# Kernel tuning notes

Hardware: AMD Instinct MI355X
Metric: run time of the kernel (lower is better)

## Reference

```python
import jax, jax.numpy as jnp
import numpy as np

B, N, DIM = 2, 512, 128
HEADS, DH = 4, 64
INNER = HEADS * DH            # 256
POS_HID = 64
MULT = 4                      # attn_mlp_hidden_mult
K = 16                        # num_neighbors


def setup_inputs() -> dict:
    key = jax.random.key(0)
    ks = jax.random.split(key, 10)
    w = lambda k, shape: jax.random.normal(k, shape, jnp.float32) * 0.02
    return {
        "x": jax.random.normal(ks[0], (B, N, DIM), jnp.float32),
        "pos": jax.random.normal(ks[1], (B, N, 3), jnp.float32),
        "mask": jnp.ones((B, N), dtype=bool),
        "w_qkv": w(ks[2], (DIM, 3 * INNER)),
        "w_out": w(ks[3], (INNER, DIM)),
        "b_out": jnp.zeros((DIM,), jnp.float32),
        "w_pos1": w(ks[4], (3, POS_HID)),
        "b_pos1": jnp.zeros((POS_HID,), jnp.float32),
        "w_pos2": w(ks[5], (POS_HID, INNER)),
        "b_pos2": jnp.zeros((INNER,), jnp.float32),
        # grouped 1x1 convs == per-head linear layers
        "w_attn1": w(ks[6], (HEADS, DH, MULT * DH)),
        "b_attn1": jnp.zeros((HEADS, MULT * DH), jnp.float32),
        "w_attn2": w(ks[7], (HEADS, MULT * DH, DH)),
        "b_attn2": jnp.zeros((HEADS, DH), jnp.float32),
    }


def reference(x, pos, mask, w_qkv, w_out, b_out, w_pos1, b_pos1, w_pos2, b_pos2,
              w_attn1, b_attn1, w_attn2, b_attn2):
    b, n, _ = x.shape
    h, d = HEADS, DH

    qkv = x @ w_qkv                                   # [b, n, 3*inner]
    q, k, v = jnp.split(qkv, 3, axis=-1)
    to_heads = lambda t: t.reshape(b, n, h, d).transpose(0, 2, 1, 3)  # b h n d
    q, k, v = map(to_heads, (q, k, v))

    # dense pairwise relative positions + pos MLP  [b, n, n, inner]
    rel_pos = pos[:, :, None, :] - pos[:, None, :, :]            # [b, n, n, 3]
    rpe = jax.nn.relu(rel_pos @ w_pos1 + b_pos1) @ w_pos2 + b_pos2

    # masked topk over pairwise distance (smallest K)
    rel_dist = jnp.linalg.norm(rel_pos, axis=-1)                 # [b, n, n]
    mask2 = mask[:, :, None] & mask[:, None, :]                  # [b, n, n]
    fmax = jnp.finfo(rel_dist.dtype).max
    rel_dist = jnp.where(mask2, rel_dist, fmax)
    _, idx = jax.lax.top_k(-rel_dist, K)                         # [b, n, K]

    # neighbor gathers (equivalent to torch batched_index_select over j)
    gather_hd = jax.vmap(lambda t, i: t[:, i, :])                # [h,n,d],[n,K] -> [h,n,K,d]
    k_nb = gather_hd(k, idx)                                     # [b, h, n, K, d]
    v_nb = gather_hd(v, idx)
    row = jnp.arange(n)[:, None]
    rpe_nb = jax.vmap(lambda r, i: r[row, i])(rpe, idx)          # [b, n, K, inner]
    rpe_nb = rpe_nb.reshape(b, n, K, h, d).transpose(0, 3, 1, 2, 4)  # [b,h,n,K,d]
    mask_nb = jax.vmap(lambda m, i: m[row, i])(mask2, idx)       # [b, n, K]

    # qk_rel gathered implicitly: (q_i - k_j)[j=idx] == q_i - k_nb
    attn_in = q[:, :, :, None, :] - k_nb + rpe_nb                # [b, h, n, K, d]

    # grouped 1x1 conv MLP == per-head MLP on last dim
    hid = jax.nn.relu(jnp.einsum('bhikd,hde->bhike', attn_in, w_attn1)
                      + b_attn1[None, :, None, None, :])
    sim = (jnp.einsum('bhike,hed->bhikd', hid, w_attn2)
           + b_attn2[None, :, None, None, :])                    # [b, h, n, K, d]

    sim = jnp.where(mask_nb[:, None, :, :, None], sim, -fmax)
    # torch: sim is [b, (h d), i, j]; softmax(dim=-2) is over i -> axis 2 here
    attn = jax.nn.softmax(sim, axis=2)

    v_full = v_nb + rpe_nb                                       # [b, h, n, K, d]
    agg = jnp.sum(attn * v_full, axis=3)                         # [b, h, n, d]
    agg = agg.transpose(0, 2, 1, 3).reshape(b, n, h * d)         # [b, n, inner]
    return agg @ w_out + b_out
```

## Files before the change

kernel.cpp:

```cpp
#include <hip/hip_runtime.h>

#define B_ 2
#define N_ 512
#define DIM_ 128
#define HEADS_ 4
#define DH_ 64
#define INNER_ 256
#define PH_ 64
#define HID2_ 256
#define KNB_ 16

typedef unsigned long long u64;
typedef unsigned int u32;
typedef unsigned short u16;
typedef __attribute__((ext_vector_type(8))) short bf16x8;
typedef __attribute__((ext_vector_type(8))) unsigned short us8;
typedef __attribute__((ext_vector_type(4))) float f32x4;

__device__ __forceinline__ float bf2f(u16 u) {
    union { float f; u32 u; } c; c.u = ((u32)u) << 16; return c.f;
}
__device__ __forceinline__ u16 f2bf(float f) {
    union { float f; u32 u; } c; c.f = f;
    u32 u = c.u;
    return (u16)((u + 0x7fffu + ((u >> 16) & 1u)) >> 16);
}
__device__ __forceinline__ u32 pack2(float lo, float hi) {
    return ((u32)f2bf(hi) << 16) | (u32)f2bf(lo);
}

__global__ __launch_bounds__(256) void k_front(
        const float* __restrict__ x, const float* __restrict__ pos, const float* __restrict__ w_qkv,
        const float* __restrict__ w_a1, const float* __restrict__ w_a2, const float* __restrict__ w_p2,
        u16* __restrict__ wf1, u16* __restrict__ wf2, u16* __restrict__ wfp,
        u16* __restrict__ qb, u16* __restrict__ kb, float* __restrict__ v,
        int* __restrict__ idx) {
    int blk = blockIdx.x;
    if (blk < 576) {
        int t = blk * 256 + threadIdx.x;
        if (t < 65536) {
            int jj = t & 7, lbig = (t >> 3) & 63, f = t >> 9;
            int s = f & 1, etL = (f >> 1) & 7, half = (f >> 4) & 1, h = f >> 5;
            int lr = lbig & 15, g = lbig >> 4;
            int d = s * 32 + g * 8 + jj, e = (half * 8 + etL) * 16 + lr;
            wf1[t] = f2bf(w_a1[((h * 64 + d) << 8) + e]);
        } else if (t < 131072) {
            int t2 = t - 65536;
            int jj = t2 & 7, lbig = (t2 >> 3) & 63, f = t2 >> 9;
            int s = f & 7, ct = (f >> 3) & 3, h = f >> 5;
            int lr = lbig & 15, g = lbig >> 4;
            int e = s * 32 + g * 8 + jj, c = ct * 16 + lr;
            wf2[t2] = f2bf(w_a2[(((h << 8) + e) << 6) + c]);
        } else {
            int t3 = t - 131072;
            int jj = t3 & 7, lbig = (t3 >> 3) & 63, f = t3 >> 9;
            int s = f & 1, ct = (f >> 1) & 3, h = f >> 3;
            int lr = lbig & 15, g = lbig >> 4;
            int e = s * 32 + g * 8 + jj, c = h * 64 + ct * 16 + lr;
            wfp[t3] = f2bf(w_p2[(e << 8) + c]);
        }
    } else if (blk < 704) {
        int bu = blk - 576;
        int b = bu >> 6;
        int n0 = (bu & 63) * 8;
        int t = threadIdx.x;
        __shared__ float xs[8][128];
        #pragma unroll
        for (int p = 0; p < 4; ++p) {
            int e = p * 256 + t;
            xs[e >> 7][e & 127] = x[((size_t)(b * N_ + n0) + (e >> 7)) * DIM_ + (e & 127)];
        }
        __syncthreads();
        float acc[3][8];
        #pragma unroll
        for (int cc = 0; cc < 3; ++cc)
            #pragma unroll
            for (int r = 0; r < 8; ++r) acc[cc][r] = 0.f;
        for (int c4 = 0; c4 < 32; ++c4) {
            float wv[3][4];
            #pragma unroll
            for (int dd = 0; dd < 4; ++dd)
                #pragma unroll
                for (int cc = 0; cc < 3; ++cc)
                    wv[cc][dd] = w_qkv[(size_t)(c4 * 4 + dd) * (3 * INNER_) + cc * INNER_ + t];
            #pragma unroll
            for (int r = 0; r < 8; ++r) {
                float4 xv = *(const float4*)&xs[r][c4 * 4];
                #pragma unroll
                for (int cc = 0; cc < 3; ++cc)
                    acc[cc][r] += xv.x * wv[cc][0] + xv.y * wv[cc][1] + xv.z * wv[cc][2] + xv.w * wv[cc][3];
            }
        }
        int h = t >> 6, d = t & 63;
        #pragma unroll
        for (int r = 0; r < 8; ++r) {
            size_t o = (((size_t)(b * HEADS_ + h)) * N_ + n0 + r) * DH_ + d;
            qb[o] = f2bf(acc[0][r]);
            kb[o] = f2bf(acc[1][r]);
            v[o]  = acc[2][r];
        }
    } else {
        int wave = (blk - 704) * 4 + (threadIdx.x >> 6);
        int lane = threadIdx.x & 63;
        int b = wave >> 9;
        float px = pos[(size_t)wave * 3 + 0];
        float py = pos[(size_t)wave * 3 + 1];
        float pz = pos[(size_t)wave * 3 + 2];
        u64 keys[8];
        #pragma unroll
        for (int s = 0; s < 8; ++s) {
            int j = s * 64 + lane;
            float dx = __fsub_rn(px, pos[(size_t)(b * N_ + j) * 3 + 0]);
            float dy = __fsub_rn(py, pos[(size_t)(b * N_ + j) * 3 + 1]);
            float dz = __fsub_rn(pz, pos[(size_t)(b * N_ + j) * 3 + 2]);
            float s2 = __fadd_rn(__fadd_rn(__fmul_rn(dx, dx), __fmul_rn(dy, dy)), __fmul_rn(dz, dz));
            float dist = __fsqrt_rn(s2);
            keys[s] = ((u64)__float_as_uint(dist) << 32) | (unsigned)j;
        }
        for (int r = 0; r < KNB_; ++r) {
            u64 m = keys[0];
            #pragma unroll
            for (int s = 1; s < 8; ++s) m = (keys[s] < m) ? keys[s] : m;
            #pragma unroll
            for (int off = 32; off >= 1; off >>= 1) {
                u64 o = __shfl_xor(m, off);
                m = (o < m) ? o : m;
            }
            if (lane == 0) idx[(size_t)wave * KNB_ + r] = (int)(m & 0xffffffffu);
            #pragma unroll
            for (int s = 0; s < 8; ++s) if (keys[s] == m) keys[s] = ~0ull;
        }
    }
}

__global__ __launch_bounds__(256, 2) void k_gather(
        const u16* __restrict__ qb, const u16* __restrict__ kb, const float* __restrict__ v,
        const int* __restrict__ idx, const float* __restrict__ pos,
        const float* __restrict__ w_p1, const float* __restrict__ b_p1,
        const float* __restrict__ b_p2, const u16* __restrict__ wfp,
        u16* __restrict__ ainb, u16* __restrict__ vf) {
    __shared__ u16 RP[4][2][16 * 72];
    int t = threadIdx.x;
    int wv = t >> 6, l = t & 63, lr = l & 15, g = l >> 4;
    int blk = blockIdx.x;
    int b = blk >> 8;
    int i0 = (blk & 255) * 2;
    int h = wv, bh = b * HEADS_ + h;

    float rx[2], ry[2], rz[2];
    us8 qv[2][2], kv[2][2];
    float4 v0[2][2], v1[2][2];
    #pragma unroll
    for (int ii = 0; ii < 2; ++ii) {
        int i = i0 + ii, bi = (b << 9) + i;
        int j = idx[(bi << 4) + lr];
        int bj = (b << 9) + j;
        rx[ii] = pos[(size_t)bi * 3 + 0] - pos[(size_t)bj * 3 + 0];
        ry[ii] = pos[(size_t)bi * 3 + 1] - pos[(size_t)bj * 3 + 1];
        rz[ii] = pos[(size_t)bi * 3 + 2] - pos[(size_t)bj * 3 + 2];
        #pragma unroll
        for (int s = 0; s < 2; ++s) {
            qv[ii][s] = *(const us8*)&qb[(size_t)(bh * N_ + i) * 64 + s * 32 + g * 8];
            kv[ii][s] = *(const us8*)&kb[(size_t)(bh * N_ + j) * 64 + s * 32 + g * 8];
            v0[ii][s] = *(const float4*)&v[(size_t)(bh * N_ + j) * 64 + s * 32 + g * 8];
            v1[ii][s] = *(const float4*)&v[(size_t)(bh * N_ + j) * 64 + s * 32 + g * 8 + 4];
        }
    }

    bf16x8 hidp[2][2];
    #pragma unroll
    for (int ii = 0; ii < 2; ++ii) {
        #pragma unroll
        for (int s = 0; s < 2; ++s) {
            u16 tmp[8];
            #pragma unroll
            for (int jj = 0; jj < 8; ++jj) {
                int e = s * 32 + g * 8 + jj;
                float hh = b_p1[e] + rx[ii] * w_p1[e] + ry[ii] * w_p1[PH_ + e] + rz[ii] * w_p1[2 * PH_ + e];
                tmp[jj] = f2bf(fmaxf(hh, 0.f));
            }
            hidp[ii][s] = *(bf16x8*)tmp;
        }
    }

    {
        bf16x8 Ar[4][2];
        #pragma unroll
        for (int ct = 0; ct < 4; ++ct)
            #pragma unroll
            for (int s = 0; s < 2; ++s)
                Ar[ct][s] = *(const bf16x8*)&wfp[(size_t)((((h << 2) + ct) << 1) + s) * 512 + l * 8];
        #pragma unroll
        for (int ct = 0; ct < 4; ++ct) {
            f32x4 C0 = {0.f, 0.f, 0.f, 0.f}, C1 = {0.f, 0.f, 0.f, 0.f};
            #pragma unroll
            for (int s = 0; s < 2; ++s) {
                C0 = __builtin_amdgcn_mfma_f32_16x16x32_bf16(Ar[ct][s], hidp[0][s], C0, 0, 0, 0);
                C1 = __builtin_amdgcn_mfma_f32_16x16x32_bf16(Ar[ct][s], hidp[1][s], C1, 0, 0, 0);
            }
            float4 bias = *(const float4*)&b_p2[h * 64 + ct * 16 + g * 4];
            uint2 o0, o1;
            o0.x = pack2(C0[0] + bias.x, C0[1] + bias.y);
            o0.y = pack2(C0[2] + bias.z, C0[3] + bias.w);
            o1.x = pack2(C1[0] + bias.x, C1[1] + bias.y);
            o1.y = pack2(C1[2] + bias.z, C1[3] + bias.w);
            *(uint2*)&RP[wv][0][lr * 72 + ct * 16 + g * 4] = o0;
            *(uint2*)&RP[wv][1][lr * 72 + ct * 16 + g * 4] = o1;
        }
    }

    #pragma unroll
    for (int ii = 0; ii < 2; ++ii) {
        int i = i0 + ii;
        #pragma unroll
        for (int s = 0; s < 2; ++s) {
            bf16x8 rp = *(const bf16x8*)&RP[wv][ii][lr * 72 + s * 32 + g * 8];
            us8 rpu = *(const us8*)&rp;
            float vvr[8] = {v0[ii][s].x, v0[ii][s].y, v0[ii][s].z, v0[ii][s].w,
                            v1[ii][s].x, v1[ii][s].y, v1[ii][s].z, v1[ii][s].w};
            u16 ta[8], tv[8];
            #pragma unroll
            for (int jj = 0; jj < 8; ++jj) {
                float rpf = bf2f(rpu[jj]);
                ta[jj] = f2bf(bf2f(qv[ii][s][jj]) - bf2f(kv[ii][s][jj]) + rpf);
                tv[jj] = f2bf(vvr[jj] + rpf);
            }
            *(bf16x8*)&ainb[((size_t)((bh * N_ + i) * 2 + s)) * 512 + l * 8] = *(bf16x8*)ta;
            *(bf16x8*)&vf[(size_t)(((bh * N_ + i) << 4) + lr) * 64 + s * 32 + g * 8] = *(bf16x8*)tv;
        }
    }
}

__global__ __launch_bounds__(256, 2) void k_mlp(
        const u16* __restrict__ ainb,
        const u16* __restrict__ wf1, const u16* __restrict__ wf2,
        const float* __restrict__ b_a1, const float* __restrict__ b_a2,
        u16* __restrict__ sim) {
    __shared__ u16 HID[4][2][16 * 136];
    int t = threadIdx.x;
    int wv = t >> 6, l = t & 63, lr = l & 15, g = l >> 4;
    int blk = blockIdx.x;
    int bh = blk >> 6;
    int h = bh & 3;
    int i0 = (blk & 63) * 8 + wv * 2;

    bf16x8 ain[2][2];
    #pragma unroll
    for (int ii = 0; ii < 2; ++ii) {
        int i = i0 + ii;
        #pragma unroll
        for (int s = 0; s < 2; ++s)
            ain[ii][s] = *(const bf16x8*)&ainb[((size_t)((bh * N_ + i) * 2 + s)) * 512 + l * 8];
    }

    f32x4 C2[2][4];
    #pragma unroll
    for (int ii = 0; ii < 2; ++ii)
        #pragma unroll
        for (int ct = 0; ct < 4; ++ct) C2[ii][ct] = (f32x4){0.f, 0.f, 0.f, 0.f};
    #pragma unroll
    for (int half = 0; half < 2; ++half) {
        bf16x8 A1[8][2];
        #pragma unroll
        for (int etL = 0; etL < 8; ++etL)
            #pragma unroll
            for (int s = 0; s < 2; ++s)
                A1[etL][s] = *(const bf16x8*)&wf1[(size_t)(((((h << 1) + half) << 3) + etL) * 2 + s) * 512 + l * 8];
        #pragma unroll
        for (int etL = 0; etL < 8; ++etL) {
            int et = half * 8 + etL;
            f32x4 C0 = {0.f, 0.f, 0.f, 0.f}, C1 = {0.f, 0.f, 0.f, 0.f};
            #pragma unroll
            for (int s = 0; s < 2; ++s) {
                C0 = __builtin_amdgcn_mfma_f32_16x16x32_bf16(A1[etL][s], ain[0][s], C0, 0, 0, 0);
                C1 = __builtin_amdgcn_mfma_f32_16x16x32_bf16(A1[etL][s], ain[1][s], C1, 0, 0, 0);
            }
            float4 bias = *(const float4*)&b_a1[h * 256 + et * 16 + g * 4];
            uint2 p0, p1;
            p0.x = pack2(fmaxf(C0[0] + bias.x, 0.f), fmaxf(C0[1] + bias.y, 0.f));
            p0.y = pack2(fmaxf(C0[2] + bias.z, 0.f), fmaxf(C0[3] + bias.w, 0.f));
            p1.x = pack2(fmaxf(C1[0] + bias.x, 0.f), fmaxf(C1[1] + bias.y, 0.f));
            p1.y = pack2(fmaxf(C1[2] + bias.z, 0.f), fmaxf(C1[3] + bias.w, 0.f));
            *(uint2*)&HID[wv][0][lr * 136 + etL * 16 + g * 4] = p0;
            *(uint2*)&HID[wv][1][lr * 136 + etL * 16 + g * 4] = p1;
        }
        #pragma unroll
        for (int chunk = 0; chunk < 2; ++chunk) {
            bf16x8 A2[4][2];
            #pragma unroll
            for (int ct = 0; ct < 4; ++ct)
                #pragma unroll
                for (int ss = 0; ss < 2; ++ss) {
                    int s = half * 4 + chunk * 2 + ss;
                    A2[ct][ss] = *(const bf16x8*)&wf2[(size_t)((((h << 2) + ct) << 3) + s) * 512 + l * 8];
                }
            #pragma unroll
            for (int ss = 0; ss < 2; ++ss) {
                int sL = chunk * 2 + ss;
                bf16x8 B0 = *(const bf16x8*)&HID[wv][0][lr * 136 + sL * 32 + g * 8];
                bf16x8 B1 = *(const bf16x8*)&HID[wv][1][lr * 136 + sL * 32 + g * 8];
                #pragma unroll
                for (int ct = 0; ct < 4; ++ct) {
                    C2[0][ct] = __builtin_amdgcn_mfma_f32_16x16x32_bf16(A2[ct][ss], B0, C2[0][ct], 0, 0, 0);
                    C2[1][ct] = __builtin_amdgcn_mfma_f32_16x16x32_bf16(A2[ct][ss], B1, C2[1][ct], 0, 0, 0);
                }
            }
        }
    }
    #pragma unroll
    for (int ii = 0; ii < 2; ++ii) {
        int i = i0 + ii;
        #pragma unroll
        for (int ct = 0; ct < 4; ++ct) {
            float4 bias = *(const float4*)&b_a2[h * 64 + ct * 16 + g * 4];
            uint2 o;
            o.x = pack2(C2[ii][ct][0] + bias.x, C2[ii][ct][1] + bias.y);
            o.y = pack2(C2[ii][ct][2] + bias.z, C2[ii][ct][3] + bias.w);
            *(uint2*)&sim[(size_t)(((bh * N_ + i) << 4) + lr) * 64 + ct * 16 + g * 4] = o;
        }
    }
}

__global__ __launch_bounds__(256) void k_stats(const u16* __restrict__ sim, float* __restrict__ P) {
    int blk = blockIdx.x;
    int half = blk & 1, ks = (blk >> 1) & 15, bh = blk >> 5;
    int d0 = (threadIdx.x & 15) * 4;
    int nc = threadIdx.x >> 4;
    __shared__ float red[16][69];
    size_t base = ((size_t)(bh * N_ + half * 256 + nc * 16) * 16 + ks) * 64 + d0;
    float s0 = 0.f, s1 = 0.f, s2 = 0.f, s3 = 0.f;
    #pragma unroll
    for (int nn = 0; nn < 16; ++nn) {
        uint2 u = *(const uint2*)&sim[base + (size_t)nn * 1024];
        s0 += __expf(bf2f((u16)(u.x & 0xffff)));
        s1 += __expf(bf2f((u16)(u.x >> 16)));
        s2 += __expf(bf2f((u16)(u.y & 0xffff)));
        s3 += __expf(bf2f((u16)(u.y >> 16)));
    }
    red[nc][d0 + 0] = s0; red[nc][d0 + 1] = s1;
    red[nc][d0 + 2] = s2; red[nc][d0 + 3] = s3;
    __syncthreads();
    int t = threadIdx.x;
    if (t < 64) {
        float s = 0.f;
        #pragma unroll
        for (int c = 0; c < 16; ++c) s += red[c][t];
        P[(size_t)blk * 64 + t] = s;
    }
}

__global__ __launch_bounds__(256) void k_agg_out(
        const u16* __restrict__ sim, const u16* __restrict__ vf, const float* __restrict__ P,
        const float* __restrict__ w, const float* __restrict__ bo, float* __restrict__ out) {
    int blk = blockIdx.x;
    int b = blk >> 8;
    int i0 = (blk & 255) * 2;
    int t = threadIdx.x;
    __shared__ float ag[2][260];
    {
        int h = t >> 6, d = t & 63;
        int bh = b * HEADS_ + h;
        float Rk[16];
        #pragma unroll
        for (int ks = 0; ks < 16; ++ks) {
            int pbase = ((bh << 5) + (ks << 1)) * 64 + d;
            Rk[ks] = 1.f / (P[pbase] + P[pbase + 64]);
        }
        #pragma unroll
        for (int r = 0; r < 2; ++r) {
            size_t base = (size_t)((bh * N_ + i0 + r) << 4) * 64 + d;
            float acc = 0.f;
            #pragma unroll
            for (int ks = 0; ks < 16; ++ks) {
                float p = __expf(bf2f(sim[base + (size_t)ks * 64])) * Rk[ks];
                acc += p * bf2f(vf[base + (size_t)ks * 64]);
            }
            ag[r][h * 64 + d] = acc;
        }
    }
    __syncthreads();
    int c = t & 127, rg = t >> 7;
    float acc = bo[c];
    for (int k4 = 0; k4 < 64; ++k4) {
        float4 a4 = *(const float4*)&ag[rg][k4 * 4];
        acc += a4.x * w[(size_t)(k4 * 4 + 0) * DIM_ + c] + a4.y * w[(size_t)(k4 * 4 + 1) * DIM_ + c]
             + a4.z * w[(size_t)(k4 * 4 + 2) * DIM_ + c] + a4.w * w[(size_t)(k4 * 4 + 3) * DIM_ + c];
    }
    out[(size_t)((b << 9) + i0 + rg) * DIM_ + c] = acc;
}

extern "C" void kernel_launch(void* const* d_in, const int* in_sizes, int n_in,
                              void* d_out, int out_size, void* d_ws, size_t ws_size,
                              hipStream_t stream) {
    const float* x      = (const float*)d_in[0];
    const float* pos    = (const float*)d_in[1];
    const float* w_qkv  = (const float*)d_in[3];
    const float* w_out  = (const float*)d_in[4];
    const float* b_out  = (const float*)d_in[5];
    const float* w_pos1 = (const float*)d_in[6];
    const float* b_pos1 = (const float*)d_in[7];
    const float* w_pos2 = (const float*)d_in[8];
    const float* b_pos2 = (const float*)d_in[9];
    const float* w_a1   = (const float*)d_in[10];
    const float* b_a1   = (const float*)d_in[11];
    const float* w_a2   = (const float*)d_in[12];
    const float* b_a2   = (const float*)d_in[13];
    float* out = (float*)d_out;

    char* W = (char*)d_ws;
    u16*  qb   = (u16*)W;            W += 524288;
    u16*  kb   = (u16*)W;            W += 524288;
    float* v   = (float*)W;          W += 1048576;
    int*  idx  = (int*)W;            W += 65536;
    u16*  sim  = (u16*)W;            W += 8388608;
    u16*  vf   = (u16*)W;            W += 8388608;
    u16*  ainb = (u16*)W;            W += 8388608;
    float* P   = (float*)W;          W += 65536;
    u16*  wf1  = (u16*)W;            W += 131072;
    u16*  wf2  = (u16*)W;            W += 131072;
    u16*  wfp  = (u16*)W;            W += 32768;

    k_front<<<960, 256, 0, stream>>>(x, pos, w_qkv, w_a1, w_a2, w_pos2,
                                     wf1, wf2, wfp, qb, kb, v, idx);
    k_gather<<<512, 256, 0, stream>>>(qb, kb, v, idx, pos, w_pos1, b_pos1, b_pos2, wfp,
                                      ainb, vf);
    k_mlp<<<512, 256, 0, stream>>>(ainb, wf1, wf2, b_a1, b_a2, sim);
    k_stats<<<256, 256, 0, stream>>>(sim, P);
    k_agg_out<<<512, 256, 0, stream>>>(sim, vf, P, w_out, b_out, out);
}
```

Before: 56.56 us.

## Fuse gather and attention-MLP kernels, keep attn input in registers, store V as bf16

Merges k_gather and k_mlp into a single k_attn kernel. The attention-MLP input is now kept in registers instead of being written to and re-read from an 8 MB global buffer, and the extra launch goes away. The block mapping changes so each block covers one (batch, head) pair with 8 query rows, and the LDS buffer is reused for both the rpe tile and the hidden activations. V is also stored as bf16 instead of fp32, halving its traffic, at some precision cost in v+rpe.

```diff
diff --git a/kernel.cpp b/kernel.cpp
--- a/kernel.cpp
+++ b/kernel.cpp
@@ -33,7 +33,7 @@
         const float* __restrict__ x, const float* __restrict__ pos, const float* __restrict__ w_qkv,
         const float* __restrict__ w_a1, const float* __restrict__ w_a2, const float* __restrict__ w_p2,
         u16* __restrict__ wf1, u16* __restrict__ wf2, u16* __restrict__ wfp,
-        u16* __restrict__ qb, u16* __restrict__ kb, float* __restrict__ v,
+        u16* __restrict__ qb, u16* __restrict__ kb, u16* __restrict__ vb,
         int* __restrict__ idx) {
     int blk = blockIdx.x;
     if (blk < 576) {
@@ -97,7 +97,7 @@
             size_t o = (((size_t)(b * HEADS_ + h)) * N_ + n0 + r) * DH_ + d;
             qb[o] = f2bf(acc[0][r]);
             kb[o] = f2bf(acc[1][r]);
-            v[o]  = acc[2][r];
+            vb[o] = f2bf(acc[2][r]);
         }
     } else {
         int wave = (blk - 704) * 4 + (threadIdx.x >> 6);
@@ -133,23 +133,24 @@
     }
 }
 
-__global__ __launch_bounds__(256, 2) void k_gather(
-        const u16* __restrict__ qb, const u16* __restrict__ kb, const float* __restrict__ v,
-        const int* __restrict__ idx, const float* __restrict__ pos,
-        const float* __restrict__ w_p1, const float* __restrict__ b_p1,
+__global__ __launch_bounds__(256, 2) void k_attn(
+        const u16* __restrict__ qb, const u16* __restrict__ kb, const u16* __restrict__ vb,
+        const int* __restrict__ idx,
+        const float* __restrict__ pos, const float* __restrict__ w_p1, const float* __restrict__ b_p1,
         const float* __restrict__ b_p2, const u16* __restrict__ wfp,
-        u16* __restrict__ ainb, u16* __restrict__ vf) {
-    __shared__ u16 RP[4][2][16 * 72];
+        const u16* __restrict__ wf1, const u16* __restrict__ wf2,
+        const float* __restrict__ b_a1, const float* __restrict__ b_a2,
+        u16* __restrict__ sim, u16* __restrict__ vf) {
+    __shared__ u16 HID[4][2][16 * 136];
     int t = threadIdx.x;
     int wv = t >> 6, l = t & 63, lr = l & 15, g = l >> 4;
     int blk = blockIdx.x;
-    int b = blk >> 8;
-    int i0 = (blk & 255) * 2;
-    int h = wv, bh = b * HEADS_ + h;
+    int bh = blk >> 6;
+    int b = bh >> 2, h = bh & 3;
+    int i0 = (blk & 63) * 8 + wv * 2;
 
     float rx[2], ry[2], rz[2];
-    us8 qv[2][2], kv[2][2];
-    float4 v0[2][2], v1[2][2];
+    us8 qv[2][2], kv[2][2], vvb[2][2];
     #pragma unroll
     for (int ii = 0; ii < 2; ++ii) {
         int i = i0 + ii, bi = (b << 9) + i;
@@ -160,10 +161,9 @@
         rz[ii] = pos[(size_t)bi * 3 + 2] - pos[(size_t)bj * 3 + 2];
         #pragma unroll
         for (int s = 0; s < 2; ++s) {
-            qv[ii][s] = *(const us8*)&qb[(size_t)(bh * N_ + i) * 64 + s * 32 + g * 8];
-            kv[ii][s] = *(const us8*)&kb[(size_t)(bh * N_ + j) * 64 + s * 32 + g * 8];
-            v0[ii][s] = *(const float4*)&v[(size_t)(bh * N_ + j) * 64 + s * 32 + g * 8];
-            v1[ii][s] = *(const float4*)&v[(size_t)(bh * N_ + j) * 64 + s * 32 + g * 8 + 4];
+            qv[ii][s]  = *(const us8*)&qb[(size_t)(bh * N_ + i) * 64 + s * 32 + g * 8];
+            kv[ii][s]  = *(const us8*)&kb[(size_t)(bh * N_ + j) * 64 + s * 32 + g * 8];
+            vvb[ii][s] = *(const us8*)&vb[(size_t)(bh * N_ + j) * 64 + s * 32 + g * 8];
         }
     }
 
@@ -204,53 +204,29 @@
             o0.y = pack2(C0[2] + bias.z, C0[3] + bias.w);
             o1.x = pack2(C1[0] + bias.x, C1[1] + bias.y);
             o1.y = pack2(C1[2] + bias.z, C1[3] + bias.w);
-            *(uint2*)&RP[wv][0][lr * 72 + ct * 16 + g * 4] = o0;
-            *(uint2*)&RP[wv][1][lr * 72 + ct * 16 + g * 4] = o1;
-        }
-    }
-
+            *(uint2*)&HID[wv][0][lr * 136 + ct * 16 + g * 4] = o0;
+            *(uint2*)&HID[wv][1][lr * 136 + ct * 16 + g * 4] = o1;
+        }
+    }
+
+    bf16x8 ain[2][2];
     #pragma unroll
     for (int ii = 0; ii < 2; ++ii) {
         int i = i0 + ii;
         #pragma unroll
         for (int s = 0; s < 2; ++s) {
-            bf16x8 rp = *(const bf16x8*)&RP[wv][ii][lr * 72 + s * 32 + g * 8];
+            bf16x8 rp = *(const bf16x8*)&HID[wv][ii][lr * 136 + s * 32 + g * 8];
             us8 rpu = *(const us8*)&rp;
-            float vvr[8] = {v0[ii][s].x, v0[ii][s].y, v0[ii][s].z, v0[ii][s].w,
-                            v1[ii][s].x, v1[ii][s].y, v1[ii][s].z, v1[ii][s].w};
             u16 ta[8], tv[8];
             #pragma unroll
             for (int jj = 0; jj < 8; ++jj) {
                 float rpf = bf2f(rpu[jj]);
                 ta[jj] = f2bf(bf2f(qv[ii][s][jj]) - bf2f(kv[ii][s][jj]) + rpf);
-                tv[jj] = f2bf(vvr[jj] + rpf);
-            }
-            *(bf16x8*)&ainb[((size_t)((bh * N_ + i) * 2 + s)) * 512 + l * 8] = *(bf16x8*)ta;
+                tv[jj] = f2bf(bf2f(vvb[ii][s][jj]) + rpf);
+            }
+            ain[ii][s] = *(bf16x8*)ta;
             *(bf16x8*)&vf[(size_t)(((bh * N_ + i) << 4) + lr) * 64 + s * 32 + g * 8] = *(bf16x8*)tv;
         }
-    }
-}
-
-__global__ __launch_bounds__(256, 2) void k_mlp(
-        const u16* __restrict__ ainb,
-        const u16* __restrict__ wf1, const u16* __restrict__ wf2,
-        const float* __restrict__ b_a1, const float* __restrict__ b_a2,
-        u16* __restrict__ sim) {
-    __shared__ u16 HID[4][2][16 * 136];
-    int t = threadIdx.x;
-    int wv = t >> 6, l = t & 63, lr = l & 15, g = l >> 4;
-    int blk = blockIdx.x;
-    int bh = blk >> 6;
-    int h = bh & 3;
-    int i0 = (blk & 63) * 8 + wv * 2;
-
-    bf16x8 ain[2][2];
-    #pragma unroll
-    for (int ii = 0; ii < 2; ++ii) {
-        int i = i0 + ii;
-        #pragma unroll
-        for (int s = 0; s < 2; ++s)
-            ain[ii][s] = *(const bf16x8*)&ainb[((size_t)((bh * N_ + i) * 2 + s)) * 512 + l * 8];
     }
 
     f32x4 C2[2][4];
@@ -410,21 +386,19 @@
     char* W = (char*)d_ws;
     u16*  qb   = (u16*)W;            W += 524288;
     u16*  kb   = (u16*)W;            W += 524288;
-    float* v   = (float*)W;          W += 1048576;
+    u16*  vb   = (u16*)W;            W += 524288;
     int*  idx  = (int*)W;            W += 65536;
     u16*  sim  = (u16*)W;            W += 8388608;
     u16*  vf   = (u16*)W;            W += 8388608;
-    u16*  ainb = (u16*)W;            W += 8388608;
     float* P   = (float*)W;          W += 65536;
     u16*  wf1  = (u16*)W;            W += 131072;
     u16*  wf2  = (u16*)W;            W += 131072;
     u16*  wfp  = (u16*)W;            W += 32768;
 
     k_front<<<960, 256, 0, stream>>>(x, pos, w_qkv, w_a1, w_a2, w_pos2,
-                                     wf1, wf2, wfp, qb, kb, v, idx);
-    k_gather<<<512, 256, 0, stream>>>(qb, kb, v, idx, pos, w_pos1, b_pos1, b_pos2, wfp,
-                                      ainb, vf);
-    k_mlp<<<512, 256, 0, stream>>>(ainb, wf1, wf2, b_a1, b_a2, sim);
+                                     wf1, wf2, wfp, qb, kb, vb, idx);
+    k_attn<<<512, 256, 0, stream>>>(qb, kb, vb, idx, pos, w_pos1, b_pos1, b_pos2, wfp,
+                                    wf1, wf2, b_a1, b_a2, sim, vf);
     k_stats<<<256, 256, 0, stream>>>(sim, P);
     k_agg_out<<<512, 256, 0, stream>>>(sim, vf, P, w_out, b_out, out);
 }
```

Measured after the change: 59.64 us. +5.4%, slower.

## Stage MLP weights and positions in LDS, store V as bf16

Applied to the files above, without the earlier changes.

k_mlp now copies the per-head wf1/wf2 weight fragments (64 KB) into shared memory once per block and reads MFMA A operands from LDS instead of from global memory per wave. k_gather stages the batch's positions in shared memory for the relative-position computation. V is stored and gathered in bf16 instead of fp32, which halves its traffic. The exchange is a large LDS footprint in k_mlp, with the min-blocks launch bound dropped, which lowers occupancy, plus extra rounding of V.

```diff
diff --git a/kernel.cpp b/kernel.cpp
--- a/kernel.cpp
+++ b/kernel.cpp
@@ -33,7 +33,7 @@
         const float* __restrict__ x, const float* __restrict__ pos, const float* __restrict__ w_qkv,
         const float* __restrict__ w_a1, const float* __restrict__ w_a2, const float* __restrict__ w_p2,
         u16* __restrict__ wf1, u16* __restrict__ wf2, u16* __restrict__ wfp,
-        u16* __restrict__ qb, u16* __restrict__ kb, float* __restrict__ v,
+        u16* __restrict__ qb, u16* __restrict__ kb, u16* __restrict__ vb,
         int* __restrict__ idx) {
     int blk = blockIdx.x;
     if (blk < 576) {
@@ -97,7 +97,7 @@
             size_t o = (((size_t)(b * HEADS_ + h)) * N_ + n0 + r) * DH_ + d;
             qb[o] = f2bf(acc[0][r]);
             kb[o] = f2bf(acc[1][r]);
-            v[o]  = acc[2][r];
+            vb[o] = f2bf(acc[2][r]);
         }
     } else {
         int wave = (blk - 704) * 4 + (threadIdx.x >> 6);
@@ -134,12 +134,13 @@
 }
 
 __global__ __launch_bounds__(256, 2) void k_gather(
-        const u16* __restrict__ qb, const u16* __restrict__ kb, const float* __restrict__ v,
+        const u16* __restrict__ qb, const u16* __restrict__ kb, const u16* __restrict__ vb,
         const int* __restrict__ idx, const float* __restrict__ pos,
         const float* __restrict__ w_p1, const float* __restrict__ b_p1,
         const float* __restrict__ b_p2, const u16* __restrict__ wfp,
         u16* __restrict__ ainb, u16* __restrict__ vf) {
     __shared__ u16 RP[4][2][16 * 72];
+    __shared__ float PSM[1536];
     int t = threadIdx.x;
     int wv = t >> 6, l = t & 63, lr = l & 15, g = l >> 4;
     int blk = blockIdx.x;
@@ -147,36 +148,40 @@
     int i0 = (blk & 255) * 2;
     int h = wv, bh = b * HEADS_ + h;
 
-    float rx[2], ry[2], rz[2];
-    us8 qv[2][2], kv[2][2];
-    float4 v0[2][2], v1[2][2];
+    #pragma unroll
+    for (int p = 0; p < 6; ++p)
+        PSM[p * 256 + t] = pos[(size_t)b * 1536 + p * 256 + t];
+
+    int jn[2];
+    us8 qv[2][2], kv[2][2], vvb[2][2];
     #pragma unroll
     for (int ii = 0; ii < 2; ++ii) {
         int i = i0 + ii, bi = (b << 9) + i;
         int j = idx[(bi << 4) + lr];
-        int bj = (b << 9) + j;
-        rx[ii] = pos[(size_t)bi * 3 + 0] - pos[(size_t)bj * 3 + 0];
-        ry[ii] = pos[(size_t)bi * 3 + 1] - pos[(size_t)bj * 3 + 1];
-        rz[ii] = pos[(size_t)bi * 3 + 2] - pos[(size_t)bj * 3 + 2];
+        jn[ii] = j;
         #pragma unroll
         for (int s = 0; s < 2; ++s) {
-            qv[ii][s] = *(const us8*)&qb[(size_t)(bh * N_ + i) * 64 + s * 32 + g * 8];
-            kv[ii][s] = *(const us8*)&kb[(size_t)(bh * N_ + j) * 64 + s * 32 + g * 8];
-            v0[ii][s] = *(const float4*)&v[(size_t)(bh * N_ + j) * 64 + s * 32 + g * 8];
-            v1[ii][s] = *(const float4*)&v[(size_t)(bh * N_ + j) * 64 + s * 32 + g * 8 + 4];
-        }
-    }
+            qv[ii][s]  = *(const us8*)&qb[(size_t)(bh * N_ + i) * 64 + s * 32 + g * 8];
+            kv[ii][s]  = *(const us8*)&kb[(size_t)(bh * N_ + j) * 64 + s * 32 + g * 8];
+            vvb[ii][s] = *(const us8*)&vb[(size_t)(bh * N_ + j) * 64 + s * 32 + g * 8];
+        }
+    }
+    __syncthreads();
 
     bf16x8 hidp[2][2];
     #pragma unroll
     for (int ii = 0; ii < 2; ++ii) {
+        int i = i0 + ii, j = jn[ii];
+        float rx = PSM[i * 3 + 0] - PSM[j * 3 + 0];
+        float ry = PSM[i * 3 + 1] - PSM[j * 3 + 1];
+        float rz = PSM[i * 3 + 2] - PSM[j * 3 + 2];
         #pragma unroll
         for (int s = 0; s < 2; ++s) {
             u16 tmp[8];
             #pragma unroll
             for (int jj = 0; jj < 8; ++jj) {
                 int e = s * 32 + g * 8 + jj;
-                float hh = b_p1[e] + rx[ii] * w_p1[e] + ry[ii] * w_p1[PH_ + e] + rz[ii] * w_p1[2 * PH_ + e];
+                float hh = b_p1[e] + rx * w_p1[e] + ry * w_p1[PH_ + e] + rz * w_p1[2 * PH_ + e];
                 tmp[jj] = f2bf(fmaxf(hh, 0.f));
             }
             hidp[ii][s] = *(bf16x8*)tmp;
@@ -216,14 +221,12 @@
         for (int s = 0; s < 2; ++s) {
             bf16x8 rp = *(const bf16x8*)&RP[wv][ii][lr * 72 + s * 32 + g * 8];
             us8 rpu = *(const us8*)&rp;
-            float vvr[8] = {v0[ii][s].x, v0[ii][s].y, v0[ii][s].z, v0[ii][s].w,
-                            v1[ii][s].x, v1[ii][s].y, v1[ii][s].z, v1[ii][s].w};
             u16 ta[8], tv[8];
             #pragma unroll
             for (int jj = 0; jj < 8; ++jj) {
                 float rpf = bf2f(rpu[jj]);
                 ta[jj] = f2bf(bf2f(qv[ii][s][jj]) - bf2f(kv[ii][s][jj]) + rpf);
-                tv[jj] = f2bf(vvr[jj] + rpf);
+                tv[jj] = f2bf(bf2f(vvb[ii][s][jj]) + rpf);
             }
             *(bf16x8*)&ainb[((size_t)((bh * N_ + i) * 2 + s)) * 512 + l * 8] = *(bf16x8*)ta;
             *(bf16x8*)&vf[(size_t)(((bh * N_ + i) << 4) + lr) * 64 + s * 32 + g * 8] = *(bf16x8*)tv;
@@ -231,11 +234,13 @@
     }
 }
 
-__global__ __launch_bounds__(256, 2) void k_mlp(
+__global__ __launch_bounds__(256) void k_mlp(
         const u16* __restrict__ ainb,
         const u16* __restrict__ wf1, const u16* __restrict__ wf2,
         const float* __restrict__ b_a1, const float* __restrict__ b_a2,
         u16* __restrict__ sim) {
+    __shared__ u16 W1[16384];
+    __shared__ u16 W2[16384];
     __shared__ u16 HID[4][2][16 * 136];
     int t = threadIdx.x;
     int wv = t >> 6, l = t & 63, lr = l & 15, g = l >> 4;
@@ -253,6 +258,18 @@
             ain[ii][s] = *(const bf16x8*)&ainb[((size_t)((bh * N_ + i) * 2 + s)) * 512 + l * 8];
     }
 
+    {
+        const u16* s1 = wf1 + ((size_t)h << 14);
+        const u16* s2 = wf2 + ((size_t)h << 14);
+        #pragma unroll
+        for (int p = 0; p < 8; ++p) {
+            int e = p * 2048 + t * 8;
+            *(bf16x8*)&W1[e] = *(const bf16x8*)&s1[e];
+            *(bf16x8*)&W2[e] = *(const bf16x8*)&s2[e];
+        }
+    }
+    __syncthreads();
+
     f32x4 C2[2][4];
     #pragma unroll
     for (int ii = 0; ii < 2; ++ii)
@@ -260,20 +277,15 @@
         for (int ct = 0; ct < 4; ++ct) C2[ii][ct] = (f32x4){0.f, 0.f, 0.f, 0.f};
     #pragma unroll
     for (int half = 0; half < 2; ++half) {
-        bf16x8 A1[8][2];
-        #pragma unroll
-        for (int etL = 0; etL < 8; ++etL)
-            #pragma unroll
-            for (int s = 0; s < 2; ++s)
-                A1[etL][s] = *(const bf16x8*)&wf1[(size_t)(((((h << 1) + half) << 3) + etL) * 2 + s) * 512 + l * 8];
         #pragma unroll
         for (int etL = 0; etL < 8; ++etL) {
             int et = half * 8 + etL;
             f32x4 C0 = {0.f, 0.f, 0.f, 0.f}, C1 = {0.f, 0.f, 0.f, 0.f};
             #pragma unroll
             for (int s = 0; s < 2; ++s) {
-                C0 = __builtin_amdgcn_mfma_f32_16x16x32_bf16(A1[etL][s], ain[0][s], C0, 0, 0, 0);
-                C1 = __builtin_amdgcn_mfma_f32_16x16x32_bf16(A1[etL][s], ain[1][s], C1, 0, 0, 0);
+                bf16x8 A = *(const bf16x8*)&W1[((((half << 3) + etL) << 1) + s) * 512 + l * 8];
+                C0 = __builtin_amdgcn_mfma_f32_16x16x32_bf16(A, ain[0][s], C0, 0, 0, 0);
+                C1 = __builtin_amdgcn_mfma_f32_16x16x32_bf16(A, ain[1][s], C1, 0, 0, 0);
             }
             float4 bias = *(const float4*)&b_a1[h * 256 + et * 16 + g * 4];
             uint2 p0, p1;
@@ -285,25 +297,15 @@
             *(uint2*)&HID[wv][1][lr * 136 + etL * 16 + g * 4] = p1;
         }
         #pragma unroll
-        for (int chunk = 0; chunk < 2; ++chunk) {
-            bf16x8 A2[4][2];
-            #pragma unroll
-            for (int ct = 0; ct < 4; ++ct)
-                #pragma unroll
-                for (int ss = 0; ss < 2; ++ss) {
-                    int s = half * 4 + chunk * 2 + ss;
-                    A2[ct][ss] = *(const bf16x8*)&wf2[(size_t)((((h << 2) + ct) << 3) + s) * 512 + l * 8];
-                }
-            #pragma unroll
-            for (int ss = 0; ss < 2; ++ss) {
-                int sL = chunk * 2 + ss;
-                bf16x8 B0 = *(const bf16x8*)&HID[wv][0][lr * 136 + sL * 32 + g * 8];
-                bf16x8 B1 = *(const bf16x8*)&HID[wv][1][lr * 136 + sL * 32 + g * 8];
-                #pragma unroll
-                for (int ct = 0; ct < 4; ++ct) {
-                    C2[0][ct] = __builtin_amdgcn_mfma_f32_16x16x32_bf16(A2[ct][ss], B0, C2[0][ct], 0, 0, 0);
-                    C2[1][ct] = __builtin_amdgcn_mfma_f32_16x16x32_bf16(A2[ct][ss], B1, C2[1][ct], 0, 0, 0);
-                }
+        for (int sL = 0; sL < 4; ++sL) {
+            int s = half * 4 + sL;
+            bf16x8 B0 = *(const bf16x8*)&HID[wv][0][lr * 136 + sL * 32 + g * 8];
+            bf16x8 B1 = *(const bf16x8*)&HID[wv][1][lr * 136 + sL * 32 + g * 8];
+            #pragma unroll
+            for (int ct = 0; ct < 4; ++ct) {
+                bf16x8 A = *(const bf16x8*)&W2[((ct << 3) + s) * 512 + l * 8];
+                C2[0][ct] = __builtin_amdgcn_mfma_f32_16x16x32_bf16(A, B0, C2[0][ct], 0, 0, 0);
+                C2[1][ct] = __builtin_amdgcn_mfma_f32_16x16x32_bf16(A, B1, C2[1][ct], 0, 0, 0);
             }
         }
     }
@@ -410,7 +412,7 @@
     char* W = (char*)d_ws;
     u16*  qb   = (u16*)W;            W += 524288;
     u16*  kb   = (u16*)W;            W += 524288;
-    float* v   = (float*)W;          W += 1048576;
+    u16*  vb   = (u16*)W;            W += 524288;
     int*  idx  = (int*)W;            W += 65536;
     u16*  sim  = (u16*)W;            W += 8388608;
     u16*  vf   = (u16*)W;            W += 8388608;
@@ -421,8 +423,8 @@
     u16*  wfp  = (u16*)W;            W += 32768;
 
     k_front<<<960, 256, 0, stream>>>(x, pos, w_qkv, w_a1, w_a2, w_pos2,
-                                     wf1, wf2, wfp, qb, kb, v, idx);
-    k_gather<<<512, 256, 0, stream>>>(qb, kb, v, idx, pos, w_pos1, b_pos1, b_pos2, wfp,
+                                     wf1, wf2, wfp, qb, kb, vb, idx);
+    k_gather<<<512, 256, 0, stream>>>(qb, kb, vb, idx, pos, w_pos1, b_pos1, b_pos2, wfp,
                                       ainb, vf);
     k_mlp<<<512, 256, 0, stream>>>(ainb, wf1, wf2, b_a1, b_a2, sim);
     k_stats<<<256, 256, 0, stream>>>(sim, P);
```

Result: slower. 59.52 us (+5.2%).
